# Kernel tuning notes

Hardware: AMD Instinct MI355X
Metric: run time of the kernel (lower is better)

## Reference

```python
import jax, jax.numpy as jnp
import numpy as np

CH = 8        # CHANNELS
CONVS = 8     # CONVOLUTIONS
HID = 32      # HIDDEN
NTYPES = 6    # NODE_TYPES
N_NODES = 200000
N_EDGES = 6400000
ENTRIES = 2048
BN_EPS = 1e-5


def setup_inputs() -> dict:
    key = jax.random.key(0)
    ks = jax.random.split(key, 12)
    x = jax.random.randint(ks[0], (N_NODES,), 0, NTYPES)
    edge_index = jax.random.randint(ks[1], (2, N_EDGES), 0, N_NODES)
    entry_index = jax.random.randint(ks[2], (ENTRIES,), 0, N_NODES)
    emb = jax.random.normal(ks[3], (NTYPES, CH), jnp.float32)
    bn_gamma = jnp.ones((CONVS, CH), jnp.float32)
    bn_beta = jnp.zeros((CONVS, CH), jnp.float32)
    conv_w = jax.random.normal(ks[4], (CONVS, CH, CH), jnp.float32) * (1.0 / np.sqrt(CH))
    conv_b = jnp.zeros((CONVS, CH), jnp.float32)
    hidden_w = jax.random.normal(ks[5], (2 * CH, HID), jnp.float32) * (1.0 / np.sqrt(2 * CH))
    hidden_b = jnp.zeros((HID,), jnp.float32)
    out_w = jax.random.normal(ks[6], (HID, 1), jnp.float32) * (1.0 / np.sqrt(HID))
    out_b = jnp.zeros((1,), jnp.float32)
    return dict(x=x, edge_index=edge_index, entry_index=entry_index, emb=emb,
                bn_gamma=bn_gamma, bn_beta=bn_beta, conv_w=conv_w, conv_b=conv_b,
                hidden_w=hidden_w, hidden_b=hidden_b, out_w=out_w, out_b=out_b)


def reference(x, edge_index, entry_index, emb, bn_gamma, bn_beta,
              conv_w, conv_b, hidden_w, hidden_b, out_w, out_b):
    N = x.shape[0]
    src, dst = edge_index[0], edge_index[1]
    # GCN symmetric normalization with self-loops (PyG gcn_norm):
    # deg[i] = 1 (self loop) + in-degree(i); norm_e = deg[src]^-1/2 * deg[dst]^-1/2
    deg = jax.ops.segment_sum(jnp.ones(src.shape[0], jnp.float32), dst, num_segments=N) + 1.0
    dinv = jax.lax.rsqrt(deg)                       # [N]
    enorm = (dinv[src] * dinv[dst])[:, None]        # [E,1]
    self_norm = (dinv * dinv)[:, None]              # [N,1] self-loop coefficient

    h = emb[x]                                      # [N,CH]
    for l in range(CONVS):
        # BatchNorm (training mode: batch statistics over nodes)
        mu = h.mean(axis=0)
        var = jnp.mean((h - mu) ** 2, axis=0)
        hn = (h - mu) * jax.lax.rsqrt(var + BN_EPS) * bn_gamma[l] + bn_beta[l]
        # GCNConv: linear transform then normalized aggregation
        ht = hn @ conv_w[l]                         # [N,CH]
        agg = jax.ops.segment_sum(ht[src] * enorm, dst, num_segments=N)
        agg = agg + ht * self_norm + conv_b[l]
        h = jax.nn.relu(h + agg)                    # residual + ReLU

    xe = h[entry_index]                             # [E,CH]
    E = xe.shape[0]
    # cartesian_prod(line, line): pair[i,j] = concat(xe[i], xe[j])
    pair = jnp.concatenate([
        jnp.broadcast_to(xe[:, None, :], (E, E, CH)),
        jnp.broadcast_to(xe[None, :, :], (E, E, CH)),
    ], axis=-1)                                     # [E,E,2CH]
    hid = jax.nn.relu(pair @ hidden_w + hidden_b)   # [E,E,HID]
    out = (hid @ out_w + out_b).reshape(E, E)
    return out
```

## Files before the change

### kernel.cpp

```cpp
#include <hip/hip_runtime.h>
#include <hip/hip_fp16.h>

#define NNODES 200000
#define NEDGES 6400000
#define NENT   2048
#define CH     8
#define HID    32
#define NCONV  8
#define BN_EPS 1e-5f

#define BSZ    512
#define NBUCK  ((NNODES + BSZ - 1) / BSZ)
#define CHUNK  4096
#define NCHUNK ((NEDGES + CHUNK - 1) / CHUNK)
#define SPAD   16

#define FXSCALE   2097152.0f
#define FXINV     (1.0f/2097152.0f)

__global__ __launch_bounds__(256) void k_chist(const int* __restrict__ dst, int* __restrict__ cnt, int E){
  __shared__ int hist[NBUCK];
  for(int t=threadIdx.x; t<NBUCK; t+=256) hist[t]=0;
  __syncthreads();
  int e0 = blockIdx.x*CHUNK;
  int n = min(CHUNK, E-e0);
  for(int i=threadIdx.x; i<n; i+=256) atomicAdd(&hist[dst[e0+i]>>9], 1);
  __syncthreads();
  for(int t=threadIdx.x; t<NBUCK; t+=256) cnt[(size_t)blockIdx.x*NBUCK + t] = hist[t];
}

__global__ __launch_bounds__(256) void k_cscan(int* __restrict__ cnt, int* __restrict__ total){
  int b = blockIdx.x;
  __shared__ int sd[256];
  int carry = 0;
  for(int base=0; base<NCHUNK; base+=256){
    int c = base + threadIdx.x;
    int v = (c<NCHUNK) ? cnt[(size_t)c*NBUCK + b] : 0;
    sd[threadIdx.x] = v; __syncthreads();
    #pragma unroll
    for(int o=1; o<256; o<<=1){
      int x = (threadIdx.x>=o) ? sd[threadIdx.x-o] : 0;
      __syncthreads();
      sd[threadIdx.x] += x;
      __syncthreads();
    }
    if(c<NCHUNK) cnt[(size_t)c*NBUCK + b] = carry + sd[threadIdx.x] - v;
    carry += sd[255];
    __syncthreads();
  }
  if(threadIdx.x==0) total[b] = carry;
}

__global__ __launch_bounds__(512) void k_bscan(const int* __restrict__ total, int* __restrict__ bbase){
  __shared__ int sd[512];
  int t = threadIdx.x;
  int v = (t<NBUCK) ? total[t] : 0;
  sd[t] = v; __syncthreads();
  #pragma unroll
  for(int o=1; o<512; o<<=1){
    int x = (t>=o) ? sd[t-o] : 0;
    __syncthreads();
    sd[t] += x;
    __syncthreads();
  }
  if(t<NBUCK) bbase[t] = sd[t] - v;
  if(t==511) bbase[NBUCK] = sd[511];
}

__global__ __launch_bounds__(512) void k_bin(const int* __restrict__ src, const int* __restrict__ dst,
                                             const int* __restrict__ cnt, const int* __restrict__ bbase,
                                             unsigned int* __restrict__ binned, int E){
  __shared__ int hist[NBUCK], excl[NBUCK], cur[NBUCK], base[NBUCK];
  __shared__ unsigned int pin[CHUNK];
  __shared__ unsigned short bk_in[CHUNK];
  __shared__ unsigned int sorted[CHUNK];
  __shared__ unsigned short sbkt[CHUNK];
  __shared__ int sd[512];
  int c = blockIdx.x;
  int e0 = c*CHUNK, n = min(CHUNK, E-e0);
  for(int t=threadIdx.x; t<NBUCK; t+=512) hist[t]=0;
  __syncthreads();
  for(int i=threadIdx.x; i<n; i+=512){
    int s = src[e0+i], d = dst[e0+i];
    int b = d>>9;
    pin[i]   = ((unsigned)(d & (BSZ-1))<<18) | (unsigned)s;
    bk_in[i] = (unsigned short)b;
    atomicAdd(&hist[b], 1);
  }
  __syncthreads();
  int t = threadIdx.x;
  int hv = (t<NBUCK) ? hist[t] : 0;
  sd[t] = hv; __syncthreads();
  #pragma unroll
  for(int o=1; o<512; o<<=1){
    int x = (t>=o) ? sd[t-o] : 0;
    __syncthreads();
    sd[t] += x;
    __syncthreads();
  }
  if(t<NBUCK){
    int ex = sd[t] - hv;
    excl[t] = ex; cur[t] = ex;
    base[t] = bbase[t] + cnt[(size_t)c*NBUCK + t];
  }
  __syncthreads();
  for(int i=threadIdx.x; i<n; i+=512){
    int b = bk_in[i];
    int slot = atomicAdd(&cur[b], 1);
    sorted[slot] = pin[i];
    sbkt[slot]   = (unsigned short)b;
  }
  __syncthreads();
  for(int i=threadIdx.x; i<n; i+=512){
    int b = sbkt[i];
    binned[ base[b] + (i - excl[b]) ] = sorted[i];
  }
}

__global__ __launch_bounds__(512) void k_sub(const unsigned int* __restrict__ binned,
                                             const int* __restrict__ bbase,
                                             unsigned int* __restrict__ binned2,
                                             float* __restrict__ dinv, int N){
  __shared__ int hd[BSZ];
  __shared__ int hs[NBUCK];
  __shared__ int cur[NBUCK];
  __shared__ int sd[512];
  int b = blockIdx.x, t = threadIdx.x;
  hd[t] = 0;
  if(t < NBUCK) hs[t] = 0;
  __syncthreads();
  int s0 = bbase[b], s1 = bbase[b+1];
  for(int i=s0+t; i<s1; i+=512){
    unsigned p = binned[i];
    atomicAdd(&hd[p>>18], 1);
    atomicAdd(&hs[(p & 0x3FFFF)>>9], 1);
  }
  __syncthreads();
  int node = b*BSZ + t;
  if(node < N) dinv[node] = 1.0f / sqrtf((float)hd[t] + 1.0f);
  int hv = (t<NBUCK) ? hs[t] : 0;
  sd[t] = hv; __syncthreads();
  #pragma unroll
  for(int o=1; o<512; o<<=1){
    int x = (t>=o) ? sd[t-o] : 0;
    __syncthreads();
    sd[t] += x;
    __syncthreads();
  }
  if(t<NBUCK) cur[t] = s0 + sd[t] - hv;
  __syncthreads();
  for(int i=s0+t; i<s1; i+=512){
    unsigned p = binned[i];
    int slot = atomicAdd(&cur[(p & 0x3FFFF)>>9], 1);
    binned2[slot] = p;
  }
}

__global__ __launch_bounds__(256) void k_init_h(const int* __restrict__ x, const float* __restrict__ emb,
                                                float* __restrict__ h, float* __restrict__ stats0, int N){
  int i = blockIdx.x*256 + threadIdx.x;
  float v[CH];
  #pragma unroll
  for(int c=0;c<CH;c++) v[c]=0.f;
  if(i < N){
    int tt = x[i];
    const float4* ep = (const float4*)(emb + (size_t)tt*CH);
    float4 a = ep[0], b = ep[1];
    float4* hp = (float4*)(h + (size_t)i*CH);
    hp[0] = a; hp[1] = b;
    v[0]=a.x; v[1]=a.y; v[2]=a.z; v[3]=a.w; v[4]=b.x; v[5]=b.y; v[6]=b.z; v[7]=b.w;
  }
  float s[CH], q[CH];
  #pragma unroll
  for(int c=0;c<CH;c++){ s[c]=v[c]; q[c]=v[c]*v[c]; }
  #pragma unroll
  for(int off=32; off>0; off>>=1){
    #pragma unroll
    for(int c=0;c<CH;c++){ s[c]+=__shfl_down(s[c],off); q[c]+=__shfl_down(q[c],off); }
  }
  __shared__ float ls[4][2*CH];
  int wave = threadIdx.x>>6, lane = threadIdx.x&63;
  if(lane==0){
    #pragma unroll
    for(int c=0;c<CH;c++){ ls[wave][c]=s[c]; ls[wave][CH+c]=q[c]; }
  }
  __syncthreads();
  if(threadIdx.x < 2*CH){
    float tsum = ls[0][threadIdx.x]+ls[1][threadIdx.x]+ls[2][threadIdx.x]+ls[3][threadIdx.x];
    unsafeAtomicAdd(&stats0[threadIdx.x*SPAD], tsum);
  }
}

__global__ __launch_bounds__(256) void k_ht(const float* __restrict__ h, const float* __restrict__ stats_l,
                                            const float* __restrict__ gamma, const float* __restrict__ beta,
                                            const float* __restrict__ convw,
                                            const float* __restrict__ dinv,
                                            __half* __restrict__ hts16, int l, int N){
  __shared__ float A[CH*CH], c0[CH], sA[CH], sT[CH];
  int t = threadIdx.x;
  if(t < CH){
    const float invN = 1.0f / (float)NNODES;
    float mu  = stats_l[t*SPAD]      * invN;
    float ex2 = stats_l[(CH+t)*SPAD] * invN;
    float var = ex2 - mu*mu;
    float r   = 1.0f / sqrtf(var + BN_EPS);
    float sc  = r * gamma[l*CH+t];
    sA[t] = sc;
    sT[t] = beta[l*CH+t] - mu*sc;
  }
  __syncthreads();
  if(t < CH*CH){
    int ci = t>>3, co = t&7;
    A[t] = sA[ci] * convw[(l*CH+ci)*CH+co];
  }
  if(t < CH){
    float a = 0.f;
    #pragma unroll
    for(int ci=0;ci<CH;ci++) a += sT[ci]*convw[(l*CH+ci)*CH+t];
    c0[t] = a;
  }
  __syncthreads();
  int i = blockIdx.x*blockDim.x + threadIdx.x;
  if(i >= N) return;
  const float4* hp = (const float4*)(h + (size_t)i*CH);
  float4 a = hp[0], b = hp[1];
  float v[CH] = {a.x,a.y,a.z,a.w,b.x,b.y,b.z,b.w};
  float o[CH];
  #pragma unroll
  for(int co=0;co<CH;co++) o[co]=c0[co];
  #pragma unroll
  for(int ci=0;ci<CH;ci++){
    float vv = v[ci];
    #pragma unroll
    for(int co=0;co<CH;co++) o[co] += vv*A[ci*CH+co];
  }
  float dn = dinv[i];
  union { __half hh[CH]; uint4 u; } pk;
  #pragma unroll
  for(int c=0;c<CH;c++) pk.hh[c] = __float2half(o[c]*dn);
  *(uint4*)(hts16 + (size_t)i*CH) = pk.u;
}

__global__ __launch_bounds__(1024) void k_push(const unsigned int* __restrict__ binned2,
                                               const int* __restrict__ bbase,
                                               const __half* __restrict__ hts16,
                                               const float* __restrict__ dinv,
                                               const float* __restrict__ convb,
                                               float* __restrict__ h, float* __restrict__ stats_next,
                                               int l, int N){
  __shared__ int acc[BSZ*CH];
  int b = blockIdx.x, t = threadIdx.x;
  for(int i=t; i<BSZ*CH; i+=1024) acc[i] = 0;
  __syncthreads();
  int s0 = bbase[b], s1 = bbase[b+1];
  int lane8 = t & 7;
  int g = t >> 3;
  for(int base = s0 + g*4; base < s1; base += 512){
    int m = s1 - base;
    if(m >= 4){
      unsigned p0 = binned2[base], p1 = binned2[base+1], p2 = binned2[base+2], p3 = binned2[base+3];
      float v0 = __half2float(hts16[(size_t)(p0 & 0x3FFFF)*CH + lane8]);
      float v1 = __half2float(hts16[(size_t)(p1 & 0x3FFFF)*CH + lane8]);
      float v2 = __half2float(hts16[(size_t)(p2 & 0x3FFFF)*CH + lane8]);
      float v3 = __half2float(hts16[(size_t)(p3 & 0x3FFFF)*CH + lane8]);
      atomicAdd(&acc[(p0>>18)*CH + lane8], __float2int_rn(v0*FXSCALE));
      atomicAdd(&acc[(p1>>18)*CH + lane8], __float2int_rn(v1*FXSCALE));
      atomicAdd(&acc[(p2>>18)*CH + lane8], __float2int_rn(v2*FXSCALE));
      atomicAdd(&acc[(p3>>18)*CH + lane8], __float2int_rn(v3*FXSCALE));
    } else {
      for(int i=0; i<m; i++){
        unsigned p = binned2[base+i];
        float v = __half2float(hts16[(size_t)(p & 0x3FFFF)*CH + lane8]);
        atomicAdd(&acc[(p>>18)*CH + lane8], __float2int_rn(v*FXSCALE));
      }
    }
  }
  __syncthreads();
  float vv[CH];
  #pragma unroll
  for(int c=0;c<CH;c++) vv[c]=0.f;
  int node = b*BSZ + t;
  if(t < BSZ && node < N){
    const int4* ar = (const int4*)(acc + t*CH);
    int4 a0 = ar[0], a1 = ar[1];
    float av[CH] = {(float)a0.x*FXINV,(float)a0.y*FXINV,(float)a0.z*FXINV,(float)a0.w*FXINV,
                    (float)a1.x*FXINV,(float)a1.y*FXINV,(float)a1.z*FXINV,(float)a1.w*FXINV};
    uint4 su = *(const uint4*)(hts16 + (size_t)node*CH);
    const __half2* sp = (const __half2*)&su;
    float sv[CH];
    #pragma unroll
    for(int j=0;j<4;j++){
      float2 f = __half22float2(sp[j]);
      sv[2*j] = f.x; sv[2*j+1] = f.y;
    }
    const float4* hp = (const float4*)(h + (size_t)node*CH);
    float4 h0 = hp[0], h1 = hp[1];
    float hv2[CH] = {h0.x,h0.y,h0.z,h0.w,h1.x,h1.y,h1.z,h1.w};
    float dn = dinv[node];
    #pragma unroll
    for(int c=0;c<CH;c++){
      float r = hv2[c] + convb[l*CH + c] + dn*(av[c] + sv[c]);
      vv[c] = fmaxf(r, 0.f);
    }
    float4* hw4 = (float4*)(h + (size_t)node*CH);
    hw4[0] = make_float4(vv[0],vv[1],vv[2],vv[3]);
    hw4[1] = make_float4(vv[4],vv[5],vv[6],vv[7]);
  }
  float s[CH], q[CH];
  #pragma unroll
  for(int c=0;c<CH;c++){ s[c]=vv[c]; q[c]=vv[c]*vv[c]; }
  #pragma unroll
  for(int off=32; off>0; off>>=1){
    #pragma unroll
    for(int c=0;c<CH;c++){ s[c]+=__shfl_down(s[c],off); q[c]+=__shfl_down(q[c],off); }
  }
  __shared__ float ls[16][2*CH];
  int wave = t>>6, lane = t&63;
  if(lane==0){
    #pragma unroll
    for(int c=0;c<CH;c++){ ls[wave][c]=s[c]; ls[wave][CH+c]=q[c]; }
  }
  __syncthreads();
  if(t < 2*CH){
    float tot = 0.f;
    #pragma unroll
    for(int w=0; w<16; w++) tot += ls[w][t];
    unsafeAtomicAdd(&stats_next[t*SPAD], tot);
  }
}

__global__ __launch_bounds__(256) void k_uv(const int* __restrict__ entry, const float* __restrict__ h,
                                            const float* __restrict__ hw, const float* __restrict__ hb,
                                            float* __restrict__ u, float* __restrict__ v){
  __shared__ float w[2*CH*HID];
  __shared__ float b[HID];
  for(int t=threadIdx.x; t<2*CH*HID; t+=256) w[t]=hw[t];
  if(threadIdx.x<HID) b[threadIdx.x]=hb[threadIdx.x];
  __syncthreads();
  int k = blockIdx.x*blockDim.x + threadIdx.x;
  if(k >= NENT) return;
  int node = entry[k];
  const float4* hp = (const float4*)(h + (size_t)node*CH);
  float4 a = hp[0], b4 = hp[1];
  float xe[CH] = {a.x,a.y,a.z,a.w,b4.x,b4.y,b4.z,b4.w};
  #pragma unroll 4
  for(int c=0;c<HID;c++){
    float uu = 0.f, vv = b[c];
    #pragma unroll
    for(int ci=0;ci<CH;ci++){
      uu += xe[ci]*w[ci*HID+c];
      vv += xe[ci]*w[(CH+ci)*HID+c];
    }
    u[(size_t)k*HID+c] = uu;
    v[(size_t)k*HID+c] = vv;
  }
}

__global__ __launch_bounds__(256) void k_pair(const float* __restrict__ u, const float* __restrict__ v,
                                              const float* __restrict__ ow, const float* __restrict__ ob,
                                              float* __restrict__ out){
  __shared__ float us[16][HID+1];
  __shared__ float vs[64][HID+1];
  __shared__ float wo[HID];
  int tid = threadIdx.x;
  int jb = blockIdx.x*64, ib = blockIdx.y*16;
  for(int t=tid; t<16*HID; t+=256) us[t>>5][t&31] = u[(size_t)(ib + (t>>5))*HID + (t&31)];
  for(int t=tid; t<64*HID; t+=256) vs[t>>5][t&31] = v[(size_t)(jb + (t>>5))*HID + (t&31)];
  if(tid<HID) wo[tid]=ow[tid];
  __syncthreads();
  int tx = tid&63, ty = tid>>6;
  float a0=0.f, a1=0.f, a2=0.f, a3=0.f;
  #pragma unroll
  for(int c=0;c<HID;c++){
    float vv = vs[tx][c];
    float w  = wo[c];
    a0 += fmaxf(us[ty   ][c]+vv, 0.f)*w;
    a1 += fmaxf(us[ty+4 ][c]+vv, 0.f)*w;
    a2 += fmaxf(us[ty+8 ][c]+vv, 0.f)*w;
    a3 += fmaxf(us[ty+12][c]+vv, 0.f)*w;
  }
  float o0 = ob[0];
  size_t base = (size_t)ib*2048 + jb + tx;
  out[base + (size_t)(ty   )*2048] = a0+o0;
  out[base + (size_t)(ty+4 )*2048] = a1+o0;
  out[base + (size_t)(ty+8 )*2048] = a2+o0;
  out[base + (size_t)(ty+12)*2048] = a3+o0;
}

extern "C" void kernel_launch(void* const* d_in, const int* in_sizes, int n_in,
                              void* d_out, int out_size, void* d_ws, size_t ws_size,
                              hipStream_t stream){
  const int*   x     = (const int*)d_in[0];
  const int*   ei    = (const int*)d_in[1];
  const int*   entry = (const int*)d_in[2];
  const float* emb   = (const float*)d_in[3];
  const float* gamma = (const float*)d_in[4];
  const float* beta  = (const float*)d_in[5];
  const float* convw = (const float*)d_in[6];
  const float* convb = (const float*)d_in[7];
  const float* hw    = (const float*)d_in[8];
  const float* hb    = (const float*)d_in[9];
  const float* ow    = (const float*)d_in[10];
  const float* ob    = (const float*)d_in[11];
  const int* srcp = ei;
  const int* dstp = ei + NEDGES;

  char* ws = (char*)d_ws;
  size_t o = 0;
  auto alloc = [&](size_t bytes){ void* p = ws + o; o += (bytes + 255) & ~(size_t)255; return p; };
  int*      cnt    = (int*)     alloc((size_t)NCHUNK*NBUCK*4);
  int*      total  = (int*)     alloc(NBUCK*4);
  int*      bbase  = (int*)     alloc((NBUCK+1)*4);
  unsigned* binned = (unsigned*)alloc((size_t)NEDGES*4);
  unsigned* binned2= (unsigned*)alloc((size_t)NEDGES*4);
  float*    dinv   = (float*)   alloc(NNODES*4);
  float*    h      = (float*)   alloc((size_t)NNODES*CH*4);
  __half*   hts16  = (__half*)  alloc((size_t)NNODES*CH*2);
  float*    stats  = (float*)   alloc((NCONV+1)*2*CH*SPAD*4);
  float*    ub     = (float*)   alloc((size_t)NENT*HID*4);
  float*    vb     = (float*)   alloc((size_t)NENT*HID*4);
  (void)ws_size; (void)in_sizes; (void)n_in; (void)out_size;

  k_chist<<<NCHUNK, 256, 0, stream>>>(dstp, cnt, NEDGES);
  k_cscan<<<NBUCK, 256, 0, stream>>>(cnt, total);
  k_bscan<<<1, 512, 0, stream>>>(total, bbase);
  k_bin  <<<NCHUNK, 512, 0, stream>>>(srcp, dstp, cnt, bbase, binned, NEDGES);
  k_sub  <<<NBUCK, 512, 0, stream>>>(binned, bbase, binned2, dinv, NNODES);

  hipMemsetAsync(stats, 0, (NCONV+1)*2*CH*SPAD*sizeof(float), stream);
  k_init_h<<<(NNODES+255)/256, 256, 0, stream>>>(x, emb, h, stats, NNODES);

  for(int l=0; l<NCONV; l++){
    k_ht  <<<(NNODES+255)/256, 256, 0, stream>>>(h, stats + (size_t)l*2*CH*SPAD, gamma, beta, convw,
                                                 dinv, hts16, l, NNODES);
    k_push<<<NBUCK, 1024, 0, stream>>>(binned2, bbase, hts16, dinv, convb, h,
                                       stats + (size_t)(l+1)*2*CH*SPAD, l, NNODES);
  }

  k_uv<<<NENT/256, 256, 0, stream>>>(entry, h, hw, hb, ub, vb);
  dim3 pg(2048/64, 2048/16);
  k_pair<<<pg, 256, 0, stream>>>(ub, vb, ow, ob, (float*)d_out);
}
```

Baseline: 573.2 us.

## Split k_sub sub-bucketing across two blocks per bucket with LDS staging

Each destination bucket in the second-level sort is now handled by two blocks, each owning half of the source sub-bins, which doubles the grid from 391 to 782 blocks. Each block scatters its half into a 48 KB shared-memory staging buffer and then writes it to binned2 contiguously instead of scattering directly to global memory. The cost is that each block reads the whole bucket input twice, and the larger shared-memory footprint may lower occupancy.

```diff
diff --git a/kernel.cpp b/kernel.cpp
--- a/kernel.cpp
+++ b/kernel.cpp
@@ -11,9 +11,11 @@
 
 #define BSZ    512
 #define NBUCK  ((NNODES + BSZ - 1) / BSZ)
+#define HB     (NBUCK/2)
 #define CHUNK  4096
 #define NCHUNK ((NEDGES + CHUNK - 1) / CHUNK)
 #define SPAD   16
+#define SUBCAP 12288
 
 #define FXSCALE   2097152.0f
 #define FXINV     (1.0f/2097152.0f)
@@ -125,19 +127,31 @@
   __shared__ int hs[NBUCK];
   __shared__ int cur[NBUCK];
   __shared__ int sd[512];
-  int b = blockIdx.x, t = threadIdx.x;
+  __shared__ int hbase_s;
+  __shared__ unsigned int stage[SUBCAP];
+  int b = blockIdx.x >> 1, half = blockIdx.x & 1;
+  int t = threadIdx.x;
   hd[t] = 0;
   if(t < NBUCK) hs[t] = 0;
   __syncthreads();
   int s0 = bbase[b], s1 = bbase[b+1];
-  for(int i=s0+t; i<s1; i+=512){
-    unsigned p = binned[i];
-    atomicAdd(&hd[p>>18], 1);
-    atomicAdd(&hs[(p & 0x3FFFF)>>9], 1);
-  }
-  __syncthreads();
-  int node = b*BSZ + t;
-  if(node < N) dinv[node] = 1.0f / sqrtf((float)hd[t] + 1.0f);
+  if(half == 0){
+    for(int i=s0+t; i<s1; i+=512){
+      unsigned p = binned[i];
+      atomicAdd(&hd[p>>18], 1);
+      atomicAdd(&hs[(p & 0x3FFFF)>>9], 1);
+    }
+  } else {
+    for(int i=s0+t; i<s1; i+=512){
+      unsigned p = binned[i];
+      atomicAdd(&hs[(p & 0x3FFFF)>>9], 1);
+    }
+  }
+  __syncthreads();
+  if(half == 0){
+    int node = b*BSZ + t;
+    if(node < N) dinv[node] = 1.0f / sqrtf((float)hd[t] + 1.0f);
+  }
   int hv = (t<NBUCK) ? hs[t] : 0;
   sd[t] = hv; __syncthreads();
   #pragma unroll
@@ -147,12 +161,36 @@
     sd[t] += x;
     __syncthreads();
   }
-  if(t<NBUCK) cur[t] = s0 + sd[t] - hv;
-  __syncthreads();
-  for(int i=s0+t; i<s1; i+=512){
-    unsigned p = binned[i];
-    int slot = atomicAdd(&cur[(p & 0x3FFFF)>>9], 1);
-    binned2[slot] = p;
+  int ex = sd[t] - hv;
+  if(t == HB) hbase_s = ex;
+  __syncthreads();
+  int lo = half ? hbase_s : 0;
+  int hi = half ? (s1 - s0) : hbase_s;
+  if(t < NBUCK) cur[t] = ex - lo;
+  __syncthreads();
+  int len = hi - lo;
+  if(len <= SUBCAP){
+    for(int i=s0+t; i<s1; i+=512){
+      unsigned p = binned[i];
+      int bin = (p & 0x3FFFF)>>9;
+      bool mine = half ? (bin >= HB) : (bin < HB);
+      if(mine){
+        int slot = atomicAdd(&cur[bin], 1);
+        stage[slot] = p;
+      }
+    }
+    __syncthreads();
+    for(int i=t; i<len; i+=512) binned2[s0 + lo + i] = stage[i];
+  } else {
+    for(int i=s0+t; i<s1; i+=512){
+      unsigned p = binned[i];
+      int bin = (p & 0x3FFFF)>>9;
+      bool mine = half ? (bin >= HB) : (bin < HB);
+      if(mine){
+        int slot = atomicAdd(&cur[bin], 1);
+        binned2[s0 + lo + slot] = p;
+      }
+    }
   }
 }
 
@@ -425,7 +463,7 @@
   k_cscan<<<NBUCK, 256, 0, stream>>>(cnt, total);
   k_bscan<<<1, 512, 0, stream>>>(total, bbase);
   k_bin  <<<NCHUNK, 512, 0, stream>>>(srcp, dstp, cnt, bbase, binned, NEDGES);
-  k_sub  <<<NBUCK, 512, 0, stream>>>(binned, bbase, binned2, dinv, NNODES);
+  k_sub  <<<NBUCK*2, 512, 0, stream>>>(binned, bbase, binned2, dinv, NNODES);
 
   hipMemsetAsync(stats, 0, (NCONV+1)*2*CH*SPAD*sizeof(float), stream);
   k_init_h<<<(NNODES+255)/256, 256, 0, stream>>>(x, emb, h, stats, NNODES);
```

Result: faster. 560.7 us (-2.2%).

## Halve destination bucket size and stage source-sorted edges in LDS

Applied to the files above, without the earlier changes.

Destination buckets shrink from 512 to 256 nodes. This doubles the block count for the binning, sub-sort and push kernels, so the binning and scan kernels move to 1024 threads and the push kernel drops to 512 threads with a smaller shared accumulator. The aim is better load balance and occupancy across CUs in the per-layer aggregation. The sub-sort kernel now scatters edges into an LDS staging buffer and then writes them out contiguously, replacing random global scatter writes; it falls back to the old direct path for oversized buckets. The risk is that hidden epilogue code in the push kernel may still assume the old thread-to-node mapping.

```diff
diff --git a/kernel.cpp b/kernel.cpp
--- a/kernel.cpp
+++ b/kernel.cpp
@@ -9,11 +9,13 @@
 #define NCONV  8
 #define BN_EPS 1e-5f
 
-#define BSZ    512
+#define BSZ    256
 #define NBUCK  ((NNODES + BSZ - 1) / BSZ)
+#define SRCB   391
 #define CHUNK  4096
 #define NCHUNK ((NEDGES + CHUNK - 1) / CHUNK)
 #define SPAD   16
+#define SUBCAP 12288
 
 #define FXSCALE   2097152.0f
 #define FXINV     (1.0f/2097152.0f)
@@ -24,7 +26,7 @@
   __syncthreads();
   int e0 = blockIdx.x*CHUNK;
   int n = min(CHUNK, E-e0);
-  for(int i=threadIdx.x; i<n; i+=256) atomicAdd(&hist[dst[e0+i]>>9], 1);
+  for(int i=threadIdx.x; i<n; i+=256) atomicAdd(&hist[dst[e0+i]>>8], 1);
   __syncthreads();
   for(int t=threadIdx.x; t<NBUCK; t+=256) cnt[(size_t)blockIdx.x*NBUCK + t] = hist[t];
 }
@@ -51,38 +53,38 @@
   if(threadIdx.x==0) total[b] = carry;
 }
 
-__global__ __launch_bounds__(512) void k_bscan(const int* __restrict__ total, int* __restrict__ bbase){
-  __shared__ int sd[512];
+__global__ __launch_bounds__(1024) void k_bscan(const int* __restrict__ total, int* __restrict__ bbase){
+  __shared__ int sd[1024];
   int t = threadIdx.x;
   int v = (t<NBUCK) ? total[t] : 0;
   sd[t] = v; __syncthreads();
   #pragma unroll
-  for(int o=1; o<512; o<<=1){
+  for(int o=1; o<1024; o<<=1){
     int x = (t>=o) ? sd[t-o] : 0;
     __syncthreads();
     sd[t] += x;
     __syncthreads();
   }
   if(t<NBUCK) bbase[t] = sd[t] - v;
-  if(t==511) bbase[NBUCK] = sd[511];
-}
-
-__global__ __launch_bounds__(512) void k_bin(const int* __restrict__ src, const int* __restrict__ dst,
-                                             const int* __restrict__ cnt, const int* __restrict__ bbase,
-                                             unsigned int* __restrict__ binned, int E){
+  if(t==1023) bbase[NBUCK] = sd[1023];
+}
+
+__global__ __launch_bounds__(1024) void k_bin(const int* __restrict__ src, const int* __restrict__ dst,
+                                              const int* __restrict__ cnt, const int* __restrict__ bbase,
+                                              unsigned int* __restrict__ binned, int E){
   __shared__ int hist[NBUCK], excl[NBUCK], cur[NBUCK], base[NBUCK];
   __shared__ unsigned int pin[CHUNK];
   __shared__ unsigned short bk_in[CHUNK];
   __shared__ unsigned int sorted[CHUNK];
   __shared__ unsigned short sbkt[CHUNK];
-  __shared__ int sd[512];
+  __shared__ int sd[1024];
   int c = blockIdx.x;
   int e0 = c*CHUNK, n = min(CHUNK, E-e0);
-  for(int t=threadIdx.x; t<NBUCK; t+=512) hist[t]=0;
-  __syncthreads();
-  for(int i=threadIdx.x; i<n; i+=512){
+  for(int t=threadIdx.x; t<NBUCK; t+=1024) hist[t]=0;
+  __syncthreads();
+  for(int i=threadIdx.x; i<n; i+=1024){
     int s = src[e0+i], d = dst[e0+i];
-    int b = d>>9;
+    int b = d>>8;
     pin[i]   = ((unsigned)(d & (BSZ-1))<<18) | (unsigned)s;
     bk_in[i] = (unsigned short)b;
     atomicAdd(&hist[b], 1);
@@ -92,7 +94,7 @@
   int hv = (t<NBUCK) ? hist[t] : 0;
   sd[t] = hv; __syncthreads();
   #pragma unroll
-  for(int o=1; o<512; o<<=1){
+  for(int o=1; o<1024; o<<=1){
     int x = (t>=o) ? sd[t-o] : 0;
     __syncthreads();
     sd[t] += x;
@@ -104,14 +106,14 @@
     base[t] = bbase[t] + cnt[(size_t)c*NBUCK + t];
   }
   __syncthreads();
-  for(int i=threadIdx.x; i<n; i+=512){
+  for(int i=threadIdx.x; i<n; i+=1024){
     int b = bk_in[i];
     int slot = atomicAdd(&cur[b], 1);
     sorted[slot] = pin[i];
     sbkt[slot]   = (unsigned short)b;
   }
   __syncthreads();
-  for(int i=threadIdx.x; i<n; i+=512){
+  for(int i=threadIdx.x; i<n; i+=1024){
     int b = sbkt[i];
     binned[ base[b] + (i - excl[b]) ] = sorted[i];
   }
@@ -122,12 +124,14 @@
                                              unsigned int* __restrict__ binned2,
                                              float* __restrict__ dinv, int N){
   __shared__ int hd[BSZ];
-  __shared__ int hs[NBUCK];
-  __shared__ int cur[NBUCK];
+  __shared__ int hs[SRCB];
+  __shared__ int cur[SRCB];
   __shared__ int sd[512];
-  int b = blockIdx.x, t = threadIdx.x;
-  hd[t] = 0;
-  if(t < NBUCK) hs[t] = 0;
+  __shared__ unsigned int stage[SUBCAP];
+  int b = blockIdx.x;
+  int t = threadIdx.x;
+  if(t < BSZ)  hd[t] = 0;
+  if(t < SRCB) hs[t] = 0;
   __syncthreads();
   int s0 = bbase[b], s1 = bbase[b+1];
   for(int i=s0+t; i<s1; i+=512){
@@ -136,9 +140,11 @@
     atomicAdd(&hs[(p & 0x3FFFF)>>9], 1);
   }
   __syncthreads();
-  int node = b*BSZ + t;
-  if(node < N) dinv[node] = 1.0f / sqrtf((float)hd[t] + 1.0f);
-  int hv = (t<NBUCK) ? hs[t] : 0;
+  if(t < BSZ){
+    int node = b*BSZ + t;
+    if(node < N) dinv[node] = 1.0f / sqrtf((float)hd[t] + 1.0f);
+  }
+  int hv = (t<SRCB) ? hs[t] : 0;
   sd[t] = hv; __syncthreads();
   #pragma unroll
   for(int o=1; o<512; o<<=1){
@@ -147,12 +153,23 @@
     sd[t] += x;
     __syncthreads();
   }
-  if(t<NBUCK) cur[t] = s0 + sd[t] - hv;
-  __syncthreads();
-  for(int i=s0+t; i<s1; i+=512){
-    unsigned p = binned[i];
-    int slot = atomicAdd(&cur[(p & 0x3FFFF)>>9], 1);
-    binned2[slot] = p;
+  if(t<SRCB) cur[t] = sd[t] - hv;
+  __syncthreads();
+  int len = s1 - s0;
+  if(len <= SUBCAP){
+    for(int i=s0+t; i<s1; i+=512){
+      unsigned p = binned[i];
+      int slot = atomicAdd(&cur[(p & 0x3FFFF)>>9], 1);
+      stage[slot] = p;
+    }
+    __syncthreads();
+    for(int i=t; i<len; i+=512) binned2[s0 + i] = stage[i];
+  } else {
+    for(int i=s0+t; i<s1; i+=512){
+      unsigned p = binned[i];
+      int slot = atomicAdd(&cur[(p & 0x3FFFF)>>9], 1);
+      binned2[s0 + slot] = p;
+    }
   }
 }
 
@@ -241,21 +258,22 @@
   *(uint4*)(hts16 + (size_t)i*CH) = pk.u;
 }
 
-__global__ __launch_bounds__(1024) void k_push(const unsigned int* __restrict__ binned2,
-                                               const int* __restrict__ bbase,
-                                               const __half* __restrict__ hts16,
-                                               const float* __restrict__ dinv,
-                                               const float* __restrict__ convb,
-                                               float* __restrict__ h, float* __restrict__ stats_next,
-                                               int l, int N){
+__global__ __launch_bounds__(512) void k_push(const unsigned int* __restrict__ binned2,
+                                              const int* __restrict__ bbase,
+                                              const __half* __restrict__ hts16,
+                                              const float* __restrict__ dinv,
+                                              const float* __restrict__ convb,
+                                              float* __restrict__ h, float* __restrict__ stats_next,
+                                              int l, int N){
   __shared__ int acc[BSZ*CH];
   int b = blockIdx.x, t = threadIdx.x;
-  for(int i=t; i<BSZ*CH; i+=1024) acc[i] = 0;
+  #pragma unroll
+  for(int i=t; i<BSZ*CH; i+=512) acc[i] = 0;
   __syncthreads();
   int s0 = bbase[b], s1 = bbase[b+1];
   int lane8 = t & 7;
   int g = t >> 3;
-  for(int base = s0 + g*4; base < s1; base += 512){
+  for(int base = s0 + g*4; base < s1; base += 256){
     int m = s1 - base;
     if(m >= 4){
       unsigned p0 = binned2[base], p1 = binned2[base+1], p2 = binned2[base+2], p3 = binned2[base+3];
@@ -314,7 +332,7 @@
     #pragma unroll
     for(int c=0;c<CH;c++){ s[c]+=__shfl_down(s[c],off); q[c]+=__shfl_down(q[c],off); }
   }
-  __shared__ float ls[16][2*CH];
+  __shared__ float ls[8][2*CH];
   int wave = t>>6, lane = t&63;
   if(lane==0){
     #pragma unroll
@@ -324,7 +342,7 @@
   if(t < 2*CH){
     float tot = 0.f;
     #pragma unroll
-    for(int w=0; w<16; w++) tot += ls[w][t];
+    for(int w=0; w<8; w++) tot += ls[w][t];
     unsafeAtomicAdd(&stats_next[t*SPAD], tot);
   }
 }
@@ -423,8 +441,8 @@
 
   k_chist<<<NCHUNK, 256, 0, stream>>>(dstp, cnt, NEDGES);
   k_cscan<<<NBUCK, 256, 0, stream>>>(cnt, total);
-  k_bscan<<<1, 512, 0, stream>>>(total, bbase);
-  k_bin  <<<NCHUNK, 512, 0, stream>>>(srcp, dstp, cnt, bbase, binned, NEDGES);
+  k_bscan<<<1, 1024, 0, stream>>>(total, bbase);
+  k_bin  <<<NCHUNK, 1024, 0, stream>>>(srcp, dstp, cnt, bbase, binned, NEDGES);
   k_sub  <<<NBUCK, 512, 0, stream>>>(binned, bbase, binned2, dinv, NNODES);
 
   hipMemsetAsync(stats, 0, (NCONV+1)*2*CH*SPAD*sizeof(float), stream);
@@ -433,8 +451,8 @@
   for(int l=0; l<NCONV; l++){
     k_ht  <<<(NNODES+255)/256, 256, 0, stream>>>(h, stats + (size_t)l*2*CH*SPAD, gamma, beta, convw,
                                                  dinv, hts16, l, NNODES);
-    k_push<<<NBUCK, 1024, 0, stream>>>(binned2, bbase, hts16, dinv, convb, h,
-                                       stats + (size_t)(l+1)*2*CH*SPAD, l, NNODES);
+    k_push<<<NBUCK, 512, 0, stream>>>(binned2, bbase, hts16, dinv, convb, h,
+                                      stats + (size_t)(l+1)*2*CH*SPAD, l, NNODES);
   }
 
   k_uv<<<NENT/256, 256, 0, stream>>>(entry, h, hw, hb, ub, vb);
```

New measurement: 617.7 us. 7.8% more time.
